# Kernel tuning notes

Measured on AMD Instinct MI355X. Metric: run time of the kernel, lower is better.

The kernel has to match this reference:

```python
import jax, jax.numpy as jnp
import numpy as np

BT, N, C, H, W = 1, 4, 64, 28, 60
ZC, YC, XC = 200, 8, 200  # grid dims (Zcam, Ycam, Xcam); voxel_shape=[200,200,8] -> Z=200, X=200, Y=8
OUT_C = 128
EPS = 1e-6


def setup_inputs() -> dict:
    key = jax.random.key(0)
    k1, k2, k3, k4 = jax.random.split(key, 4)
    # normalized sampling coords in ~[-1.2, 1.2] so some points fall outside the image (zero-padded)
    voxcam_coords = jax.random.uniform(k1, (BT, N, ZC, YC, XC, 3), jnp.float32, -1.2, 1.2)
    # binary visibility mask per voxel-camera pair
    vox_valid = (jax.random.uniform(k2, (BT, N, ZC, YC, XC, 1)) < 0.5).astype(jnp.float32)
    img_feats = jax.random.normal(k3, (BT, N, C, H, W), jnp.float32)
    W_comp = jax.random.normal(k4, (OUT_C, C * YC), jnp.float32) * 0.02  # MLP-as-1x1-conv height compressor
    b_comp = jnp.zeros((OUT_C,), jnp.float32)
    return {"voxcam_coords": voxcam_coords, "vox_valid": vox_valid, "img_feats": img_feats,
            "W_comp": W_comp, "b_comp": b_comp}


def _grid_sample_3d(feat, grid):
    """Trilinear grid_sample, align_corners=False, zeros padding.
    feat: (B, C, D, H, W); grid: (B, P, 3) with (x, y, z) in [-1, 1]. Returns (B, C, P)."""
    B, Cc, D, Hh, Ww = feat.shape
    x = ((grid[..., 0] + 1.0) * Ww - 1.0) * 0.5
    y = ((grid[..., 1] + 1.0) * Hh - 1.0) * 0.5
    z = ((grid[..., 2] + 1.0) * D - 1.0) * 0.5
    x0f, y0f, z0f = jnp.floor(x), jnp.floor(y), jnp.floor(z)
    wx, wy, wz = x - x0f, y - y0f, z - z0f
    x0, y0, z0 = x0f.astype(jnp.int32), y0f.astype(jnp.int32), z0f.astype(jnp.int32)

    def sample_one(fb, x0b, y0b, z0b, wxb, wyb, wzb):
        out = jnp.zeros((Cc, x0b.shape[0]), fb.dtype)
        for dz in (0, 1):
            for dy in (0, 1):
                for dx in (0, 1):
                    zi, yi, xi = z0b + dz, y0b + dy, x0b + dx
                    valid = ((zi >= 0) & (zi < D) & (yi >= 0) & (yi < Hh)
                             & (xi >= 0) & (xi < Ww)).astype(fb.dtype)
                    v = fb[:, jnp.clip(zi, 0, D - 1), jnp.clip(yi, 0, Hh - 1), jnp.clip(xi, 0, Ww - 1)]
                    w = ((wxb if dx else 1.0 - wxb) * (wyb if dy else 1.0 - wyb)
                         * (wzb if dz else 1.0 - wzb)) * valid
                    out = out + v * w[None]
        return out

    return jax.vmap(sample_one)(feat, x0, y0, z0, wx, wy, wz)


def reference(voxcam_coords, vox_valid, img_feats, W_comp, b_comp):
    bt, n, zc, yc, xc, _ = voxcam_coords.shape
    c, h, w = img_feats.shape[2], img_feats.shape[3], img_feats.shape[4]
    P = zc * yc * xc
    grid = voxcam_coords.reshape(bt * n, P, 3)
    feat = img_feats.reshape(bt * n, c, 1, h, w)  # N_group=1 depth axis
    sampled = _grid_sample_3d(feat, grid).reshape(bt, n, c, zc, yc, xc)
    mask = jnp.transpose(vox_valid, (0, 1, 5, 2, 3, 4))  # (bt, n, 1, zc, yc, xc)
    vox_feats = sampled * mask                      # get_feats_dense_grid_sample masking
    # reduce_cams: masked mean over cameras (dim=1)
    red = (vox_feats * mask).sum(axis=1) / (mask.sum(axis=1) + EPS)  # (bt, c, zc, yc, xc)
    # height compressor: 'bt c z y x -> bt (c y) z x' then 1x1 conv (MLP)
    comp_in = jnp.transpose(red, (0, 1, 3, 2, 4)).reshape(bt, c * yc, zc, xc)
    out = jnp.einsum('bczx,oc->bozx', comp_in, W_comp) + b_comp[None, :, None, None]
    # _unpack_batch: (b*t, C, Z, X) -> (b, t, C, Z, X) with b=t=1
    return out.reshape(1, bt, out.shape[1], zc, xc)
```

## Files before the change

### kernel.cpp

```cpp
#include <hip/hip_runtime.h>
#include <hip/hip_bf16.h>
#include <hip/hip_fp16.h>

#define N_  4
#define C_  64
#define H_  28
#define W_  60
#define ZC_ 200
#define YC_ 8
#define XC_ 200
#define OUTC_ 128
#define KD_ 512
#define EPS_ 1e-6f
#define ZB 4
#define XB 8
#define NCOL 32

typedef __attribute__((ext_vector_type(8))) short short8;
typedef __attribute__((ext_vector_type(4))) float f32x4;

__device__ __forceinline__ unsigned short f2bf(float f) {
    unsigned int u = __float_as_uint(f);
    u += 0x7FFF + ((u >> 16) & 1);
    return (unsigned short)(u >> 16);
}

__global__ void gsvt_prep(const float* __restrict__ img,
                          const float* __restrict__ Wc,
                          unsigned short* __restrict__ featB,
                          unsigned short* __restrict__ Wb) {
    int tid = blockIdx.x * blockDim.x + threadIdx.x;
    int stride = gridDim.x * blockDim.x;
    const int totF = N_ * H_ * W_ * C_;
    for (int i = tid; i < totF; i += stride) {
        int c  = i & 63;
        int hw = i >> 6;
        int w  = hw % W_;
        int nh = hw / W_;
        int h  = nh % H_;
        int n  = nh / H_;
        featB[i] = f2bf(img[((n * C_ + c) * H_ + h) * W_ + w]);
    }
    const int totW = OUTC_ * KD_;
    for (int i = tid; i < totW; i += stride) {
        int k = i & (KD_ - 1);
        int o = i >> 9;
        int y = k >> 6;
        int c = k & 63;
        Wb[i] = f2bf(Wc[o * KD_ + c * YC_ + y]);
    }
}

__device__ __forceinline__ void accp(float2* n, const uint4 V, const float w) {
    float2 f0, f1, f2, f3;
    f0.x = __uint_as_float(V.x << 16); f0.y = __uint_as_float(V.x & 0xFFFF0000u);
    f1.x = __uint_as_float(V.y << 16); f1.y = __uint_as_float(V.y & 0xFFFF0000u);
    f2.x = __uint_as_float(V.z << 16); f2.y = __uint_as_float(V.z & 0xFFFF0000u);
    f3.x = __uint_as_float(V.w << 16); f3.y = __uint_as_float(V.w & 0xFFFF0000u);
    n[0].x += w * f0.x; n[0].y += w * f0.y;
    n[1].x += w * f1.x; n[1].y += w * f1.y;
    n[2].x += w * f2.x; n[2].y += w * f2.y;
    n[3].x += w * f3.x; n[3].y += w * f3.y;
}

__global__ __launch_bounds__(256, 3) void gsvt_fused1p(
        const float* __restrict__ coords,
        const float* __restrict__ validm,
        const unsigned short* __restrict__ featB,
        const unsigned short* __restrict__ Wb,
        const float* __restrict__ bias,
        float* __restrict__ out)
{
    __shared__ uint4 tab[N_ * 256];
    __shared__ unsigned short redB[64][NCOL][8];
    float (*ms)[4] = (float(*)[4])&redB[0][0][0];

    const int z0 = blockIdx.y * ZB;
    const int x0 = blockIdx.x * XB;
    const int t  = threadIdx.x;

    const int p0   = t;
    const int y0_  = t >> 5;
    const int col0 = t & 31;
    const int zg   = z0 + (col0 >> 3);
    const int xg   = x0 + (col0 & 7);

    float gx[4], gy[4], gzv[4], mm[4];
    #pragma unroll
    for (int cam = 0; cam < N_; ++cam) {
        const int cb = ((cam * ZC_ + zg) * YC_ + y0_) * XC_ + xg;
        gx[cam]  = coords[cb * 3 + 0];
        gy[cam]  = coords[cb * 3 + 1];
        gzv[cam] = coords[cb * 3 + 2];
        mm[cam]  = validm[cb];
        ms[p0][cam] = mm[cam];
    }
    __syncthreads();

    {
        const float inv = 1.0f / (ms[p0][0] + ms[p0][1] + ms[p0][2] + ms[p0][3] + EPS_);
        #pragma unroll
        for (int cam = 0; cam < N_; ++cam) {
            const float xf = ((gx[cam] + 1.0f) * (float)W_ - 1.0f) * 0.5f;
            const float yf = ((gy[cam] + 1.0f) * (float)H_ - 1.0f) * 0.5f;
            const float zf = gzv[cam] * 0.5f;
            const float x0f = floorf(xf), y0f = floorf(yf), z0f = floorf(zf);
            const float wx = xf - x0f, wy = yf - y0f, wz = zf - z0f;
            const int xi = (int)x0f, yi = (int)y0f, zi = (int)z0f;

            const float zw = (zi == 0) ? (1.f - wz) : ((zi == -1) ? wz : 0.f);
            const float s  = mm[cam] * zw * inv;

            const float wx0 = (xi >= 0 && xi < W_)         ? (1.f - wx) * s : 0.f;
            const float wx1 = (xi + 1 >= 0 && xi + 1 < W_) ? wx * s         : 0.f;
            const float wy0 = (yi >= 0 && yi < H_)         ? (1.f - wy)     : 0.f;
            const float wy1 = (yi + 1 >= 0 && yi + 1 < H_) ? wy             : 0.f;

            const float w00 = wy0 * wx0, w01 = wy0 * wx1;
            const float w10 = wy1 * wx0, w11 = wy1 * wx1;

            const unsigned hlo = (unsigned)__half_as_ushort(__float2half_rn(w00))
                               | ((unsigned)__half_as_ushort(__float2half_rn(w01)) << 16);
            const unsigned hhi = (unsigned)__half_as_ushort(__float2half_rn(w10))
                               | ((unsigned)__half_as_ushort(__float2half_rn(w11)) << 16);

            const int xc0 = min(max(xi, 0), W_ - 1);
            const int xc1 = min(max(xi + 1, 0), W_ - 1);
            const int yc0 = min(max(yi, 0), H_ - 1);
            const int yc1 = min(max(yi + 1, 0), H_ - 1);
            const unsigned base = (unsigned)((((cam * H_ + yc0) * W_) + xc0) * 128);
            const unsigned dxo  = (unsigned)((xc1 - xc0) * 128);
            const unsigned dyo  = (unsigned)((yc1 - yc0) * W_ * 128);
            tab[cam * 256 + p0] = make_uint4(hlo, hhi, base, dxo | (dyo << 16));
        }
    }
    __syncthreads();

    const int grp   = t >> 3;
    const int lane8 = t & 7;
    const unsigned lb = (unsigned)(lane8 << 4);
    const char* fb = (const char*)featB;

    #pragma unroll
    for (int y = 0; y < YC_; ++y) {
        const int p = y * 32 + grp;

        float2 num[4] = {{0.f,0.f},{0.f,0.f},{0.f,0.f},{0.f,0.f}};

        #pragma unroll
        for (int cam = 0; cam < N_; ++cam) {
            const uint4 T = tab[cam * 256 + p];
            if (T.x | T.y) {
                const float2 wlo = __half22float2(*(const __half2*)&T.x);
                const float2 whi = __half22float2(*(const __half2*)&T.y);
                const unsigned base = T.z + lb;
                const unsigned dxo = T.w & 0xFFFFu;
                const unsigned dyo = T.w >> 16;
                const uint4 V0 = *(const uint4*)(fb + base);
                const uint4 V1 = *(const uint4*)(fb + (base + dxo));
                const uint4 V2 = *(const uint4*)(fb + (base + dyo));
                const uint4 V3 = *(const uint4*)(fb + (base + dyo + dxo));
                accp(num, V0, wlo.x);
                accp(num, V1, wlo.y);
                accp(num, V2, whi.x);
                accp(num, V3, whi.y);
            }
        }

        unsigned r0, r1, r2, r3;
        asm("v_cvt_pk_bf16_f32 %0, %1, %2" : "=v"(r0) : "v"(num[0].x), "v"(num[0].y));
        asm("v_cvt_pk_bf16_f32 %0, %1, %2" : "=v"(r1) : "v"(num[1].x), "v"(num[1].y));
        asm("v_cvt_pk_bf16_f32 %0, %1, %2" : "=v"(r2) : "v"(num[2].x), "v"(num[2].y));
        asm("v_cvt_pk_bf16_f32 %0, %1, %2" : "=v"(r3) : "v"(num[3].x), "v"(num[3].y));

        const int kb   = y * 8 + lane8;
        const int pcol = (grp & 16) | ((grp ^ kb) & 15);
        *(uint4*)&redB[kb][pcol][0] = make_uint4(r0, r1, r2, r3);
    }
    __syncthreads();

    const int wave = t >> 6;
    const int lane = t & 63;
    const int q    = lane >> 4;
    const int l16  = lane & 15;

    f32x4 acc00 = {0.f,0.f,0.f,0.f}, acc01 = {0.f,0.f,0.f,0.f};
    f32x4 acc10 = {0.f,0.f,0.f,0.f}, acc11 = {0.f,0.f,0.f,0.f};
    const unsigned short* wbase = Wb + (wave * 32 + l16) * KD_;

    #pragma unroll
    for (int ks = 0; ks < 16; ++ks) {
        const int kb = ks * 4 + q;
        const int xs = l16 ^ (kb & 15);
        const short8 B0 = *(const short8*)&redB[kb][xs][0];
        const short8 B1 = *(const short8*)&redB[kb][16 + xs][0];
        const short8 A0 = *(const short8*)(wbase + ks * 32 + q * 8);
        const short8 A1 = *(const short8*)(wbase + 16 * KD_ + ks * 32 + q * 8);
        acc00 = __builtin_amdgcn_mfma_f32_16x16x32_bf16(A0, B0, acc00, 0, 0, 0);
        acc01 = __builtin_amdgcn_mfma_f32_16x16x32_bf16(A0, B1, acc01, 0, 0, 0);
        acc10 = __builtin_amdgcn_mfma_f32_16x16x32_bf16(A1, B0, acc10, 0, 0, 0);
        acc11 = __builtin_amdgcn_mfma_f32_16x16x32_bf16(A1, B1, acc11, 0, 0, 0);
    }

    #pragma unroll
    for (int ct = 0; ct < 2; ++ct) {
        const int col = ct * 16 + l16;
        const int zz  = col >> 3;
        const int xl  = col & 7;
        const int ob  = (z0 + zz) * XC_ + x0 + xl;
        const f32x4 a0 = ct ? acc01 : acc00;
        const f32x4 a1 = ct ? acc11 : acc10;
        #pragma unroll
        for (int j = 0; j < 4; ++j) {
            const int o0 = wave * 32 + q * 4 + j;
            out[o0 * (ZC_ * XC_) + ob] = a0[j] + bias[o0];
            const int o1 = o0 + 16;
            out[o1 * (ZC_ * XC_) + ob] = a1[j] + bias[o1];
        }
    }
}

extern "C" void kernel_launch(void* const* d_in, const int* in_sizes, int n_in,
                              void* d_out, int out_size, void* d_ws, size_t ws_size,
                              hipStream_t stream) {
    const float* coords = (const float*)d_in[0];
    const float* validm = (const float*)d_in[1];
    const float* img    = (const float*)d_in[2];
    const float* Wc     = (const float*)d_in[3];
    const float* bias   = (const float*)d_in[4];
    float* out = (float*)d_out;

    unsigned short* featB = (unsigned short*)d_ws;
    unsigned short* Wb    = featB + (N_ * H_ * W_ * C_);

    gsvt_prep<<<512, 256, 0, stream>>>(img, Wc, featB, Wb);

    dim3 grid(XC_ / XB, ZC_ / ZB);
    gsvt_fused1p<<<grid, 256, 0, stream>>>(coords, validm, featB, Wb, bias, out);
}
```

Measured before the change: 63.95 us.

## Compress sample table to 8 bytes and skip inactive cameras via bitmask

Shrinks each per-voxel-camera table entry from 16 to 8 bytes by quantising the four bilinear weights to 12 bits and packing the pixel index and neighbour offsets into bit fields. Builds a per-column bitmask of cameras with nonzero weight using shared-memory atomics, so the gather loop visits only active cameras instead of testing each one. Raises the launch-bounds occupancy hint from 3 to 4 blocks, relying on the smaller shared footprint. The 12-bit weight quantisation lowers accuracy compared with fp16 weights.

```diff
diff --git a/kernel.cpp b/kernel.cpp
--- a/kernel.cpp
+++ b/kernel.cpp
@@ -63,7 +63,7 @@
     n[3].x += w * f3.x; n[3].y += w * f3.y;
 }
 
-__global__ __launch_bounds__(256, 3) void gsvt_fused1p(
+__global__ __launch_bounds__(256, 4) void gsvt_fused2(
         const float* __restrict__ coords,
         const float* __restrict__ validm,
         const unsigned short* __restrict__ featB,
@@ -71,9 +71,10 @@
         const float* __restrict__ bias,
         float* __restrict__ out)
 {
-    __shared__ uint4 tab[N_ * 256];
+    __shared__ uint2 tab2[N_ * 256];
     __shared__ unsigned short redB[64][NCOL][8];
     float (*ms)[4] = (float(*)[4])&redB[0][0][0];
+    unsigned* cmaskA = (unsigned*)((char*)&redB[0][0][0] + 4096);
 
     const int z0 = blockIdx.y * ZB;
     const int x0 = blockIdx.x * XB;
@@ -84,6 +85,8 @@
     const int col0 = t & 31;
     const int zg   = z0 + (col0 >> 3);
     const int xg   = x0 + (col0 & 7);
+
+    if (t < NCOL) cmaskA[t] = 0u;
 
     float gx[4], gy[4], gzv[4], mm[4];
     #pragma unroll
@@ -116,66 +119,77 @@
             const float wy0 = (yi >= 0 && yi < H_)         ? (1.f - wy)     : 0.f;
             const float wy1 = (yi + 1 >= 0 && yi + 1 < H_) ? wy             : 0.f;
 
-            const float w00 = wy0 * wx0, w01 = wy0 * wx1;
-            const float w10 = wy1 * wx0, w11 = wy1 * wx1;
-
-            const unsigned hlo = (unsigned)__half_as_ushort(__float2half_rn(w00))
-                               | ((unsigned)__half_as_ushort(__float2half_rn(w01)) << 16);
-            const unsigned hhi = (unsigned)__half_as_ushort(__float2half_rn(w10))
-                               | ((unsigned)__half_as_ushort(__float2half_rn(w11)) << 16);
+            const unsigned q00 = (unsigned)(wy0 * wx0 * 4095.f + 0.5f);
+            const unsigned q01 = (unsigned)(wy0 * wx1 * 4095.f + 0.5f);
+            const unsigned q10 = (unsigned)(wy1 * wx0 * 4095.f + 0.5f);
+            const unsigned q11 = (unsigned)(wy1 * wx1 * 4095.f + 0.5f);
 
             const int xc0 = min(max(xi, 0), W_ - 1);
             const int xc1 = min(max(xi + 1, 0), W_ - 1);
             const int yc0 = min(max(yi, 0), H_ - 1);
             const int yc1 = min(max(yi + 1, 0), H_ - 1);
-            const unsigned base = (unsigned)((((cam * H_ + yc0) * W_) + xc0) * 128);
-            const unsigned dxo  = (unsigned)((xc1 - xc0) * 128);
-            const unsigned dyo  = (unsigned)((yc1 - yc0) * W_ * 128);
-            tab[cam * 256 + p0] = make_uint4(hlo, hhi, base, dxo | (dyo << 16));
+            const unsigned pixidx = (unsigned)((cam * H_ + yc0) * W_ + xc0);
+            const unsigned fdx = (unsigned)(xc1 - xc0);
+            const unsigned fdy = (unsigned)(yc1 - yc0);
+
+            const unsigned A = q00 | (q01 << 12) | ((q10 & 0xFFu) << 24);
+            const unsigned B = (q10 >> 8) | (q11 << 4) | (pixidx << 16)
+                             | (fdx << 29) | (fdy << 30);
+            tab2[cam * 256 + p0] = make_uint2(A, B);
+
+            if (q00 | q01 | q10 | q11)
+                atomicOr(&cmaskA[col0], 1u << (y0_ * 4 + cam));
         }
     }
     __syncthreads();
 
     const int grp   = t >> 3;
     const int lane8 = t & 7;
+    const unsigned cm = cmaskA[grp];
+    __syncthreads();
+
     const unsigned lb = (unsigned)(lane8 << 4);
     const char* fb = (const char*)featB;
 
     #pragma unroll
     for (int y = 0; y < YC_; ++y) {
-        const int p = y * 32 + grp;
-
-        float2 num[4] = {{0.f,0.f},{0.f,0.f},{0.f,0.f},{0.f,0.f}};
-
-        #pragma unroll
-        for (int cam = 0; cam < N_; ++cam) {
-            const uint4 T = tab[cam * 256 + p];
-            if (T.x | T.y) {
-                const float2 wlo = __half22float2(*(const __half2*)&T.x);
-                const float2 whi = __half22float2(*(const __half2*)&T.y);
-                const unsigned base = T.z + lb;
-                const unsigned dxo = T.w & 0xFFFFu;
-                const unsigned dyo = T.w >> 16;
+        const int p    = y * 32 + grp;
+        const int kb   = y * 8 + lane8;
+        const int pcol = (grp & 16) | ((grp ^ kb) & 15);
+
+        unsigned sub = (cm >> (y * 4)) & 0xFu;
+        uint4 R = make_uint4(0u, 0u, 0u, 0u);
+
+        if (sub) {
+            float2 num[4] = {{0.f,0.f},{0.f,0.f},{0.f,0.f},{0.f,0.f}};
+            while (sub) {
+                const int cam = __builtin_ctz(sub);
+                sub &= sub - 1u;
+                const uint2 T = tab2[cam * 256 + p];
+                const float w00 = (float)(T.x & 0xFFFu)                      * (1.f/4095.f);
+                const float w01 = (float)((T.x >> 12) & 0xFFFu)              * (1.f/4095.f);
+                const float w10 = (float)((T.x >> 24) | ((T.y & 0xFu) << 8)) * (1.f/4095.f);
+                const float w11 = (float)((T.y >> 4) & 0xFFFu)               * (1.f/4095.f);
+                const unsigned base = (((T.y >> 16) & 0x1FFFu) << 7) + lb;
+                const unsigned dxo  = ((T.y >> 29) & 1u) << 7;
+                const unsigned dyo  = ((T.y >> 30) & 1u) * (unsigned)(W_ * 128);
                 const uint4 V0 = *(const uint4*)(fb + base);
                 const uint4 V1 = *(const uint4*)(fb + (base + dxo));
                 const uint4 V2 = *(const uint4*)(fb + (base + dyo));
                 const uint4 V3 = *(const uint4*)(fb + (base + dyo + dxo));
-                accp(num, V0, wlo.x);
-                accp(num, V1, wlo.y);
-                accp(num, V2, whi.x);
-                accp(num, V3, whi.y);
+                accp(num, V0, w00);
+                accp(num, V1, w01);
+                accp(num, V2, w10);
+                accp(num, V3, w11);
             }
+            unsigned r0, r1, r2, r3;
+            asm("v_cvt_pk_bf16_f32 %0, %1, %2" : "=v"(r0) : "v"(num[0].x), "v"(num[0].y));
+            asm("v_cvt_pk_bf16_f32 %0, %1, %2" : "=v"(r1) : "v"(num[1].x), "v"(num[1].y));
+            asm("v_cvt_pk_bf16_f32 %0, %1, %2" : "=v"(r2) : "v"(num[2].x), "v"(num[2].y));
+            asm("v_cvt_pk_bf16_f32 %0, %1, %2" : "=v"(r3) : "v"(num[3].x), "v"(num[3].y));
+            R = make_uint4(r0, r1, r2, r3);
         }
-
-        unsigned r0, r1, r2, r3;
-        asm("v_cvt_pk_bf16_f32 %0, %1, %2" : "=v"(r0) : "v"(num[0].x), "v"(num[0].y));
-        asm("v_cvt_pk_bf16_f32 %0, %1, %2" : "=v"(r1) : "v"(num[1].x), "v"(num[1].y));
-        asm("v_cvt_pk_bf16_f32 %0, %1, %2" : "=v"(r2) : "v"(num[2].x), "v"(num[2].y));
-        asm("v_cvt_pk_bf16_f32 %0, %1, %2" : "=v"(r3) : "v"(num[3].x), "v"(num[3].y));
-
-        const int kb   = y * 8 + lane8;
-        const int pcol = (grp & 16) | ((grp ^ kb) & 15);
-        *(uint4*)&redB[kb][pcol][0] = make_uint4(r0, r1, r2, r3);
+        *(uint4*)&redB[kb][pcol][0] = R;
     }
     __syncthreads();
 
@@ -236,5 +250,5 @@
     gsvt_prep<<<512, 256, 0, stream>>>(img, Wc, featB, Wb);
 
     dim3 grid(XC_ / XB, ZC_ / ZB);
-    gsvt_fused1p<<<grid, 256, 0, stream>>>(coords, validm, featB, Wb, bias, out);
-}
+    gsvt_fused2<<<grid, 256, 0, stream>>>(coords, validm, featB, Wb, bias, out);
+}
```

After: 56.12 us. 12.3% less time.

## Replace shared-memory sample table with wave-local shuffles and packed 12-bit weights

Applied to the files above, without the earlier changes.

Each wave now owns one z-slice, so the per-point sampling table is built in registers and passed to the gathering lanes with __shfl. This removes the shared tab array and two __syncthreads. Bilinear weights are packed as 12-bit fixed point together with the pixel index in two 32-bit words, and the sparse-skip branch is dropped so all 16 gathers per y are issued up front. The kernel also asks for 4 blocks per SM. The cost is lower weight precision, extra shuffle and bit-unpack ALU work, unconditional loads for zero-weight samples, and higher register pressure from holding 16 uint4 values at once.

```diff
diff --git a/kernel.cpp b/kernel.cpp
--- a/kernel.cpp
+++ b/kernel.cpp
@@ -63,7 +63,7 @@
     n[3].x += w * f3.x; n[3].y += w * f3.y;
 }
 
-__global__ __launch_bounds__(256, 3) void gsvt_fused1p(
+__global__ __launch_bounds__(256, 4) void gsvt_fusedR(
         const float* __restrict__ coords,
         const float* __restrict__ validm,
         const unsigned short* __restrict__ featB,
@@ -71,100 +71,114 @@
         const float* __restrict__ bias,
         float* __restrict__ out)
 {
-    __shared__ uint4 tab[N_ * 256];
     __shared__ unsigned short redB[64][NCOL][8];
-    float (*ms)[4] = (float(*)[4])&redB[0][0][0];
 
     const int z0 = blockIdx.y * ZB;
     const int x0 = blockIdx.x * XB;
     const int t  = threadIdx.x;
-
-    const int p0   = t;
-    const int y0_  = t >> 5;
-    const int col0 = t & 31;
-    const int zg   = z0 + (col0 >> 3);
-    const int xg   = x0 + (col0 & 7);
-
-    float gx[4], gy[4], gzv[4], mm[4];
+    const int wv = t >> 6;
+    const int l  = t & 63;
+
+    const int yp = l >> 3;
+    const int xp = l & 7;
+    const int zs = z0 + wv;
+    const int xg = x0 + xp;
+
+    float gxv[4], gyv[4], gzv[4], mmv[4];
     #pragma unroll
     for (int cam = 0; cam < N_; ++cam) {
-        const int cb = ((cam * ZC_ + zg) * YC_ + y0_) * XC_ + xg;
-        gx[cam]  = coords[cb * 3 + 0];
-        gy[cam]  = coords[cb * 3 + 1];
+        const int cb = ((cam * ZC_ + zs) * YC_ + yp) * XC_ + xg;
+        gxv[cam] = coords[cb * 3 + 0];
+        gyv[cam] = coords[cb * 3 + 1];
         gzv[cam] = coords[cb * 3 + 2];
-        mm[cam]  = validm[cb];
-        ms[p0][cam] = mm[cam];
-    }
-    __syncthreads();
-
-    {
-        const float inv = 1.0f / (ms[p0][0] + ms[p0][1] + ms[p0][2] + ms[p0][3] + EPS_);
-        #pragma unroll
-        for (int cam = 0; cam < N_; ++cam) {
-            const float xf = ((gx[cam] + 1.0f) * (float)W_ - 1.0f) * 0.5f;
-            const float yf = ((gy[cam] + 1.0f) * (float)H_ - 1.0f) * 0.5f;
-            const float zf = gzv[cam] * 0.5f;
-            const float x0f = floorf(xf), y0f = floorf(yf), z0f = floorf(zf);
-            const float wx = xf - x0f, wy = yf - y0f, wz = zf - z0f;
-            const int xi = (int)x0f, yi = (int)y0f, zi = (int)z0f;
-
-            const float zw = (zi == 0) ? (1.f - wz) : ((zi == -1) ? wz : 0.f);
-            const float s  = mm[cam] * zw * inv;
-
-            const float wx0 = (xi >= 0 && xi < W_)         ? (1.f - wx) * s : 0.f;
-            const float wx1 = (xi + 1 >= 0 && xi + 1 < W_) ? wx * s         : 0.f;
-            const float wy0 = (yi >= 0 && yi < H_)         ? (1.f - wy)     : 0.f;
-            const float wy1 = (yi + 1 >= 0 && yi + 1 < H_) ? wy             : 0.f;
-
-            const float w00 = wy0 * wx0, w01 = wy0 * wx1;
-            const float w10 = wy1 * wx0, w11 = wy1 * wx1;
-
-            const unsigned hlo = (unsigned)__half_as_ushort(__float2half_rn(w00))
-                               | ((unsigned)__half_as_ushort(__float2half_rn(w01)) << 16);
-            const unsigned hhi = (unsigned)__half_as_ushort(__float2half_rn(w10))
-                               | ((unsigned)__half_as_ushort(__float2half_rn(w11)) << 16);
-
-            const int xc0 = min(max(xi, 0), W_ - 1);
-            const int xc1 = min(max(xi + 1, 0), W_ - 1);
-            const int yc0 = min(max(yi, 0), H_ - 1);
-            const int yc1 = min(max(yi + 1, 0), H_ - 1);
-            const unsigned base = (unsigned)((((cam * H_ + yc0) * W_) + xc0) * 128);
-            const unsigned dxo  = (unsigned)((xc1 - xc0) * 128);
-            const unsigned dyo  = (unsigned)((yc1 - yc0) * W_ * 128);
-            tab[cam * 256 + p0] = make_uint4(hlo, hhi, base, dxo | (dyo << 16));
-        }
-    }
-    __syncthreads();
-
-    const int grp   = t >> 3;
-    const int lane8 = t & 7;
+        mmv[cam] = validm[cb];
+    }
+    const float inv = 1.0f / (mmv[0] + mmv[1] + mmv[2] + mmv[3] + EPS_);
+
+    unsigned Tx[4], Ty[4];
+    #pragma unroll
+    for (int cam = 0; cam < N_; ++cam) {
+        const float xf = ((gxv[cam] + 1.0f) * (float)W_ - 1.0f) * 0.5f;
+        const float yf = ((gyv[cam] + 1.0f) * (float)H_ - 1.0f) * 0.5f;
+        const float zf = gzv[cam] * 0.5f;
+        const float x0f = floorf(xf), y0f = floorf(yf), z0f = floorf(zf);
+        const float wx = xf - x0f, wy = yf - y0f, wz = zf - z0f;
+        const int xi = (int)x0f, yi = (int)y0f, zi = (int)z0f;
+
+        const float zw = (zi == 0) ? (1.f - wz) : ((zi == -1) ? wz : 0.f);
+        const float s  = mmv[cam] * zw * inv;
+
+        const float wx0 = (xi >= 0 && xi < W_)         ? (1.f - wx) * s : 0.f;
+        const float wx1 = (xi + 1 >= 0 && xi + 1 < W_) ? wx * s         : 0.f;
+        const float wy0 = (yi >= 0 && yi < H_)         ? (1.f - wy)     : 0.f;
+        const float wy1 = (yi + 1 >= 0 && yi + 1 < H_) ? wy             : 0.f;
+
+        const unsigned q00 = (unsigned)(wy0 * wx0 * 4095.f + 0.5f);
+        const unsigned q01 = (unsigned)(wy0 * wx1 * 4095.f + 0.5f);
+        const unsigned q10 = (unsigned)(wy1 * wx0 * 4095.f + 0.5f);
+        const unsigned q11 = (unsigned)(wy1 * wx1 * 4095.f + 0.5f);
+
+        const int xc0 = min(max(xi, 0), W_ - 1);
+        const int xc1 = min(max(xi + 1, 0), W_ - 1);
+        const int yc0 = min(max(yi, 0), H_ - 1);
+        const int yc1 = min(max(yi + 1, 0), H_ - 1);
+        const unsigned pixidx = (unsigned)((cam * H_ + yc0) * W_ + xc0);
+        const unsigned fdx = (unsigned)(xc1 - xc0);
+        const unsigned fdy = (unsigned)(yc1 - yc0);
+
+        Tx[cam] = q00 | (q01 << 12) | ((q10 & 0xFFu) << 24);
+        Ty[cam] = (q10 >> 8) | (q11 << 4) | (pixidx << 16)
+                | (fdx << 29) | (fdy << 30);
+    }
+
+    const int g     = l >> 3;
+    const int lane8 = l & 7;
     const unsigned lb = (unsigned)(lane8 << 4);
-    const char* fb = (const char*)featB;
+    const int col   = wv * 8 + g;
+    const char* fb  = (const char*)featB;
 
     #pragma unroll
     for (int y = 0; y < YC_; ++y) {
-        const int p = y * 32 + grp;
+        const int idx = (y << 3) | g;
+
+        int ax[4], ay[4];
+        #pragma unroll
+        for (int cam = 0; cam < N_; ++cam) {
+            ax[cam] = __shfl((int)Tx[cam], idx);
+            ay[cam] = __shfl((int)Ty[cam], idx);
+        }
+
+        unsigned baseA[4], dxoA[4], dyoA[4];
+        #pragma unroll
+        for (int cam = 0; cam < N_; ++cam) {
+            const unsigned B = (unsigned)ay[cam];
+            baseA[cam] = (((B >> 16) & 0x1FFFu) << 7) + lb;
+            dxoA[cam]  = ((B >> 29) & 1u) << 7;
+            dyoA[cam]  = ((B >> 30) & 1u) * (unsigned)(W_ * 128);
+        }
+
+        uint4 V[4][4];
+        #pragma unroll
+        for (int cam = 0; cam < N_; ++cam) {
+            V[cam][0] = *(const uint4*)(fb + baseA[cam]);
+            V[cam][1] = *(const uint4*)(fb + (baseA[cam] + dxoA[cam]));
+            V[cam][2] = *(const uint4*)(fb + (baseA[cam] + dyoA[cam]));
+            V[cam][3] = *(const uint4*)(fb + (baseA[cam] + dyoA[cam] + dxoA[cam]));
+        }
 
         float2 num[4] = {{0.f,0.f},{0.f,0.f},{0.f,0.f},{0.f,0.f}};
-
-        #pragma unroll
-        for (int cam = 0; cam < N_; ++cam) {
-            const uint4 T = tab[cam * 256 + p];
-            if (T.x | T.y) {
-                const float2 wlo = __half22float2(*(const __half2*)&T.x);
-                const float2 whi = __half22float2(*(const __half2*)&T.y);
-                const unsigned base = T.z + lb;
-                const unsigned dxo = T.w & 0xFFFFu;
-                const unsigned dyo = T.w >> 16;
-                const uint4 V0 = *(const uint4*)(fb + base);
-                const uint4 V1 = *(const uint4*)(fb + (base + dxo));
-                const uint4 V2 = *(const uint4*)(fb + (base + dyo));
-                const uint4 V3 = *(const uint4*)(fb + (base + dyo + dxo));
-                accp(num, V0, wlo.x);
-                accp(num, V1, wlo.y);
-                accp(num, V2, whi.x);
-                accp(num, V3, whi.y);
-            }
+        #pragma unroll
+        for (int cam = 0; cam < N_; ++cam) {
+            const unsigned A = (unsigned)ax[cam];
+            const unsigned B = (unsigned)ay[cam];
+            const float w00 = (float)(A & 0xFFFu)                      * (1.f/4095.f);
+            const float w01 = (float)((A >> 12) & 0xFFFu)              * (1.f/4095.f);
+            const float w10 = (float)((A >> 24) | ((B & 0xFu) << 8))   * (1.f/4095.f);
+            const float w11 = (float)((B >> 4) & 0xFFFu)               * (1.f/4095.f);
+            accp(num, V[cam][0], w00);
+            accp(num, V[cam][1], w01);
+            accp(num, V[cam][2], w10);
+            accp(num, V[cam][3], w11);
         }
 
         unsigned r0, r1, r2, r3;
@@ -174,7 +188,7 @@
         asm("v_cvt_pk_bf16_f32 %0, %1, %2" : "=v"(r3) : "v"(num[3].x), "v"(num[3].y));
 
         const int kb   = y * 8 + lane8;
-        const int pcol = (grp & 16) | ((grp ^ kb) & 15);
+        const int pcol = (col & 16) | ((col ^ kb) & 15);
         *(uint4*)&redB[kb][pcol][0] = make_uint4(r0, r1, r2, r3);
     }
     __syncthreads();
@@ -204,9 +218,9 @@
 
     #pragma unroll
     for (int ct = 0; ct < 2; ++ct) {
-        const int col = ct * 16 + l16;
-        const int zz  = col >> 3;
-        const int xl  = col & 7;
+        const int c2  = ct * 16 + l16;
+        const int zz  = c2 >> 3;
+        const int xl  = c2 & 7;
         const int ob  = (z0 + zz) * XC_ + x0 + xl;
         const f32x4 a0 = ct ? acc01 : acc00;
         const f32x4 a1 = ct ? acc11 : acc10;
@@ -236,5 +250,5 @@
     gsvt_prep<<<512, 256, 0, stream>>>(img, Wc, featB, Wb);
 
     dim3 grid(XC_ / XB, ZC_ / ZB);
-    gsvt_fused1p<<<grid, 256, 0, stream>>>(coords, validm, featB, Wb, bias, out);
-}
+    gsvt_fusedR<<<grid, 256, 0, stream>>>(coords, validm, featB, Wb, bias, out);
+}
```

Measured after the change: 56.73 us. -11.3%, faster.

## Switch gather to fp16 packed FMA with corner-split lanes and shuffle reduction

Applied to the files above, without the earlier changes.

Features and weights are stored as fp16 instead of bf16, and the sampling phase is restructured so each group of lanes handles one bilinear corner with packed half2 FMAs. Partial sums are then combined across corner lanes with xor-shuffles, and the GEMM uses the fp16 MFMA. The aim is more memory-level parallelism per lane (one load per corner per lane) and cheaper packed arithmetic than the fp32 unpack-and-accumulate path. The cost is fp16 accumulation precision, extra shuffles, and only a quarter of the lanes writing to LDS.

```diff
diff --git a/kernel.cpp b/kernel.cpp
--- a/kernel.cpp
+++ b/kernel.cpp
@@ -16,19 +16,13 @@
 #define XB 8
 #define NCOL 32
 
-typedef __attribute__((ext_vector_type(8))) short short8;
+typedef __attribute__((ext_vector_type(8))) _Float16 half8;
 typedef __attribute__((ext_vector_type(4))) float f32x4;
-
-__device__ __forceinline__ unsigned short f2bf(float f) {
-    unsigned int u = __float_as_uint(f);
-    u += 0x7FFF + ((u >> 16) & 1);
-    return (unsigned short)(u >> 16);
-}
 
 __global__ void gsvt_prep(const float* __restrict__ img,
                           const float* __restrict__ Wc,
-                          unsigned short* __restrict__ featB,
-                          unsigned short* __restrict__ Wb) {
+                          __half* __restrict__ featH,
+                          __half* __restrict__ WbH) {
     int tid = blockIdx.x * blockDim.x + threadIdx.x;
     int stride = gridDim.x * blockDim.x;
     const int totF = N_ * H_ * W_ * C_;
@@ -39,7 +33,7 @@
         int nh = hw / W_;
         int h  = nh % H_;
         int n  = nh / H_;
-        featB[i] = f2bf(img[((n * C_ + c) * H_ + h) * W_ + w]);
+        featH[i] = __float2half(img[((n * C_ + c) * H_ + h) * W_ + w]);
     }
     const int totW = OUTC_ * KD_;
     for (int i = tid; i < totW; i += stride) {
@@ -47,27 +41,15 @@
         int o = i >> 9;
         int y = k >> 6;
         int c = k & 63;
-        Wb[i] = f2bf(Wc[o * KD_ + c * YC_ + y]);
+        WbH[i] = __float2half(Wc[o * KD_ + c * YC_ + y]);
     }
 }
 
-__device__ __forceinline__ void accp(float2* n, const uint4 V, const float w) {
-    float2 f0, f1, f2, f3;
-    f0.x = __uint_as_float(V.x << 16); f0.y = __uint_as_float(V.x & 0xFFFF0000u);
-    f1.x = __uint_as_float(V.y << 16); f1.y = __uint_as_float(V.y & 0xFFFF0000u);
-    f2.x = __uint_as_float(V.z << 16); f2.y = __uint_as_float(V.z & 0xFFFF0000u);
-    f3.x = __uint_as_float(V.w << 16); f3.y = __uint_as_float(V.w & 0xFFFF0000u);
-    n[0].x += w * f0.x; n[0].y += w * f0.y;
-    n[1].x += w * f1.x; n[1].y += w * f1.y;
-    n[2].x += w * f2.x; n[2].y += w * f2.y;
-    n[3].x += w * f3.x; n[3].y += w * f3.y;
-}
-
-__global__ __launch_bounds__(256, 3) void gsvt_fused1p(
+__global__ __launch_bounds__(256, 3) void gsvt_fusedQ(
         const float* __restrict__ coords,
         const float* __restrict__ validm,
-        const unsigned short* __restrict__ featB,
-        const unsigned short* __restrict__ Wb,
+        const __half* __restrict__ featH,
+        const __half* __restrict__ WbH,
         const float* __restrict__ bias,
         float* __restrict__ out)
 {
@@ -116,13 +98,10 @@
             const float wy0 = (yi >= 0 && yi < H_)         ? (1.f - wy)     : 0.f;
             const float wy1 = (yi + 1 >= 0 && yi + 1 < H_) ? wy             : 0.f;
 
-            const float w00 = wy0 * wx0, w01 = wy0 * wx1;
-            const float w10 = wy1 * wx0, w11 = wy1 * wx1;
-
-            const unsigned hlo = (unsigned)__half_as_ushort(__float2half_rn(w00))
-                               | ((unsigned)__half_as_ushort(__float2half_rn(w01)) << 16);
-            const unsigned hhi = (unsigned)__half_as_ushort(__float2half_rn(w10))
-                               | ((unsigned)__half_as_ushort(__float2half_rn(w11)) << 16);
+            const unsigned h00 = __half_as_ushort(__float2half(wy0 * wx0));
+            const unsigned h01 = __half_as_ushort(__float2half(wy0 * wx1));
+            const unsigned h10 = __half_as_ushort(__float2half(wy1 * wx0));
+            const unsigned h11 = __half_as_ushort(__float2half(wy1 * wx1));
 
             const int xc0 = min(max(xi, 0), W_ - 1);
             const int xc1 = min(max(xi + 1, 0), W_ - 1);
@@ -131,51 +110,81 @@
             const unsigned base = (unsigned)((((cam * H_ + yc0) * W_) + xc0) * 128);
             const unsigned dxo  = (unsigned)((xc1 - xc0) * 128);
             const unsigned dyo  = (unsigned)((yc1 - yc0) * W_ * 128);
-            tab[cam * 256 + p0] = make_uint4(hlo, hhi, base, dxo | (dyo << 16));
+            tab[cam * 256 + p0] = make_uint4(h00 | (h01 << 16), h10 | (h11 << 16),
+                                             base, dxo | (dyo << 16));
         }
     }
     __syncthreads();
 
-    const int grp   = t >> 3;
-    const int lane8 = t & 7;
+    const int wv    = t >> 6;
+    const int l     = t & 63;
+    const int hh    = l >> 5;
+    const int cr    = (l >> 3) & 3;
+    const int lane8 = l & 7;
     const unsigned lb = (unsigned)(lane8 << 4);
-    const char* fb = (const char*)featB;
-
-    #pragma unroll
-    for (int y = 0; y < YC_; ++y) {
-        const int p = y * 32 + grp;
-
-        float2 num[4] = {{0.f,0.f},{0.f,0.f},{0.f,0.f},{0.f,0.f}};
-
-        #pragma unroll
-        for (int cam = 0; cam < N_; ++cam) {
-            const uint4 T = tab[cam * 256 + p];
-            if (T.x | T.y) {
-                const float2 wlo = __half22float2(*(const __half2*)&T.x);
-                const float2 whi = __half22float2(*(const __half2*)&T.y);
-                const unsigned base = T.z + lb;
-                const unsigned dxo = T.w & 0xFFFFu;
-                const unsigned dyo = T.w >> 16;
-                const uint4 V0 = *(const uint4*)(fb + base);
-                const uint4 V1 = *(const uint4*)(fb + (base + dxo));
-                const uint4 V2 = *(const uint4*)(fb + (base + dyo));
-                const uint4 V3 = *(const uint4*)(fb + (base + dyo + dxo));
-                accp(num, V0, wlo.x);
-                accp(num, V1, wlo.y);
-                accp(num, V2, whi.x);
-                accp(num, V3, whi.y);
+    const char* fb  = (const char*)featH;
+    const int pbase = wv * 64;
+
+    #pragma unroll
+    for (int i = 0; i < 32; ++i) {
+        const int p = pbase + 2 * i + hh;
+
+        uint4 T0 = tab[0 * 256 + p];
+        uint4 T1 = tab[1 * 256 + p];
+        uint4 T2 = tab[2 * 256 + p];
+        uint4 T3 = tab[3 * 256 + p];
+
+        uint4 V0 = make_uint4(0,0,0,0), V1 = V0, V2 = V0, V3 = V0;
+        #define QLOAD(Vv, Tv)                                                  \
+            if (Tv.x | Tv.y) {                                                 \
+                const unsigned doff =                                          \
+                    ((cr & 1) ? (Tv.w & 0xFFFFu) : 0u) +                       \
+                    ((cr & 2) ? (Tv.w >> 16)     : 0u);                        \
+                Vv = *(const uint4*)(fb + Tv.z + doff + lb);                   \
             }
+        QLOAD(V0, T0) QLOAD(V1, T1) QLOAD(V2, T2) QLOAD(V3, T3)
+        #undef QLOAD
+
+        __half2 num0 = __half2half2(__ushort_as_half(0));
+        __half2 num1 = num0, num2 = num0, num3 = num0;
+        #define QACC(Vv, Tv)                                                   \
+            if (Tv.x | Tv.y) {                                                 \
+                const unsigned ww = (cr & 2) ? Tv.y : Tv.x;                    \
+                const unsigned ws = (cr & 1) ? (ww >> 16) : (ww & 0xFFFFu);    \
+                const unsigned wp = ws | (ws << 16);                           \
+                const __half2 w2 = *(const __half2*)&wp;                       \
+                num0 = __hfma2(w2, *(const __half2*)&Vv.x, num0);              \
+                num1 = __hfma2(w2, *(const __half2*)&Vv.y, num1);              \
+                num2 = __hfma2(w2, *(const __half2*)&Vv.z, num2);              \
+                num3 = __hfma2(w2, *(const __half2*)&Vv.w, num3);              \
+            }
+        QACC(V0, T0) QACC(V1, T1) QACC(V2, T2) QACC(V3, T3)
+        #undef QACC
+
+        unsigned u0 = *(unsigned*)&num0, u1 = *(unsigned*)&num1;
+        unsigned u2 = *(unsigned*)&num2, u3 = *(unsigned*)&num3;
+        #define BFLY(mask)                                                     \
+            {                                                                  \
+                unsigned s0 = __shfl_xor((int)u0, mask);                       \
+                unsigned s1 = __shfl_xor((int)u1, mask);                       \
+                unsigned s2 = __shfl_xor((int)u2, mask);                       \
+                unsigned s3 = __shfl_xor((int)u3, mask);                       \
+                __half2 a;                                                     \
+                a = __hadd2(*(__half2*)&u0, *(__half2*)&s0); u0 = *(unsigned*)&a; \
+                a = __hadd2(*(__half2*)&u1, *(__half2*)&s1); u1 = *(unsigned*)&a; \
+                a = __hadd2(*(__half2*)&u2, *(__half2*)&s2); u2 = *(unsigned*)&a; \
+                a = __hadd2(*(__half2*)&u3, *(__half2*)&s3); u3 = *(unsigned*)&a; \
+            }
+        BFLY(8) BFLY(16)
+        #undef BFLY
+
+        if (cr == 0) {
+            const int yy   = p >> 5;
+            const int colp = p & 31;
+            const int kb   = yy * 8 + lane8;
+            const int pcol = (colp & 16) | ((colp ^ kb) & 15);
+            *(uint4*)&redB[kb][pcol][0] = make_uint4(u0, u1, u2, u3);
         }
-
-        unsigned r0, r1, r2, r3;
-        asm("v_cvt_pk_bf16_f32 %0, %1, %2" : "=v"(r0) : "v"(num[0].x), "v"(num[0].y));
-        asm("v_cvt_pk_bf16_f32 %0, %1, %2" : "=v"(r1) : "v"(num[1].x), "v"(num[1].y));
-        asm("v_cvt_pk_bf16_f32 %0, %1, %2" : "=v"(r2) : "v"(num[2].x), "v"(num[2].y));
-        asm("v_cvt_pk_bf16_f32 %0, %1, %2" : "=v"(r3) : "v"(num[3].x), "v"(num[3].y));
-
-        const int kb   = y * 8 + lane8;
-        const int pcol = (grp & 16) | ((grp ^ kb) & 15);
-        *(uint4*)&redB[kb][pcol][0] = make_uint4(r0, r1, r2, r3);
     }
     __syncthreads();
 
@@ -186,27 +195,27 @@
 
     f32x4 acc00 = {0.f,0.f,0.f,0.f}, acc01 = {0.f,0.f,0.f,0.f};
     f32x4 acc10 = {0.f,0.f,0.f,0.f}, acc11 = {0.f,0.f,0.f,0.f};
-    const unsigned short* wbase = Wb + (wave * 32 + l16) * KD_;
+    const __half* wbase = WbH + (wave * 32 + l16) * KD_;
 
     #pragma unroll
     for (int ks = 0; ks < 16; ++ks) {
         const int kb = ks * 4 + q;
         const int xs = l16 ^ (kb & 15);
-        const short8 B0 = *(const short8*)&redB[kb][xs][0];
-        const short8 B1 = *(const short8*)&redB[kb][16 + xs][0];
-        const short8 A0 = *(const short8*)(wbase + ks * 32 + q * 8);
-        const short8 A1 = *(const short8*)(wbase + 16 * KD_ + ks * 32 + q * 8);
-        acc00 = __builtin_amdgcn_mfma_f32_16x16x32_bf16(A0, B0, acc00, 0, 0, 0);
-        acc01 = __builtin_amdgcn_mfma_f32_16x16x32_bf16(A0, B1, acc01, 0, 0, 0);
-        acc10 = __builtin_amdgcn_mfma_f32_16x16x32_bf16(A1, B0, acc10, 0, 0, 0);
-        acc11 = __builtin_amdgcn_mfma_f32_16x16x32_bf16(A1, B1, acc11, 0, 0, 0);
+        const half8 B0 = *(const half8*)&redB[kb][xs][0];
+        const half8 B1 = *(const half8*)&redB[kb][16 + xs][0];
+        const half8 A0 = *(const half8*)(wbase + ks * 32 + q * 8);
+        const half8 A1 = *(const half8*)(wbase + 16 * KD_ + ks * 32 + q * 8);
+        acc00 = __builtin_amdgcn_mfma_f32_16x16x32_f16(A0, B0, acc00, 0, 0, 0);
+        acc01 = __builtin_amdgcn_mfma_f32_16x16x32_f16(A0, B1, acc01, 0, 0, 0);
+        acc10 = __builtin_amdgcn_mfma_f32_16x16x32_f16(A1, B0, acc10, 0, 0, 0);
+        acc11 = __builtin_amdgcn_mfma_f32_16x16x32_f16(A1, B1, acc11, 0, 0, 0);
     }
 
     #pragma unroll
     for (int ct = 0; ct < 2; ++ct) {
-        const int col = ct * 16 + l16;
-        const int zz  = col >> 3;
-        const int xl  = col & 7;
+        const int c2  = ct * 16 + l16;
+        const int zz  = c2 >> 3;
+        const int xl  = c2 & 7;
         const int ob  = (z0 + zz) * XC_ + x0 + xl;
         const f32x4 a0 = ct ? acc01 : acc00;
         const f32x4 a1 = ct ? acc11 : acc10;
@@ -230,11 +239,11 @@
     const float* bias   = (const float*)d_in[4];
     float* out = (float*)d_out;
 
-    unsigned short* featB = (unsigned short*)d_ws;
-    unsigned short* Wb    = featB + (N_ * H_ * W_ * C_);
-
-    gsvt_prep<<<512, 256, 0, stream>>>(img, Wc, featB, Wb);
+    __half* featH = (__half*)d_ws;
+    __half* WbH   = featH + (N_ * H_ * W_ * C_);
+
+    gsvt_prep<<<512, 256, 0, stream>>>(img, Wc, featH, WbH);
 
     dim3 grid(XC_ / XB, ZC_ / ZB);
-    gsvt_fused1p<<<grid, 256, 0, stream>>>(coords, validm, featB, Wb, bias, out);
+    gsvt_fusedQ<<<grid, 256, 0, stream>>>(coords, validm, featH, WbH, bias, out);
 }
```

Measured after the change: 69.48 us. +8.6%, slower.
